# Performance work log

Measured on AMD Instinct MI355X. Metric: run time of the kernel, lower is better.

## Reference

```python
import jax, jax.numpy as jnp
import numpy as np

# Levi-Civita tensor for the 1e x 1e -> 1e CG path (component normalization: eps/sqrt(2))
_e = np.zeros((3, 3, 3), dtype=np.float32)
_e[0, 1, 2] = _e[1, 2, 0] = _e[2, 0, 1] = 1.0
_e[0, 2, 1] = _e[2, 1, 0] = _e[1, 0, 2] = -1.0
EPS = jnp.asarray(_e)

B = 400000
M1S, M1V = 16, 8    # site irreps: 16x0e + 8x1e
MES, MEV = 4, 4     # edge irreps: 4x0e + 4x1e


def _split(x, mul_s, mul_v):
    # flat e3nn layout: scalars first, then vectors (xyz blocks)
    return x[:, :mul_s], x[:, mul_s:].reshape(x.shape[0], mul_v, 3)


def _fctp(x0, x1, y0, y1, W00, W11_0, W01, W10, W11_1):
    """FullyConnectedTensorProduct over irreps {0e,1e} x {0e,1e} -> {0e,1e}.
    x0:[B,u], x1:[B,u,3], y0:[B,v], y1:[B,v,3]."""
    fan0 = W00.shape[0] * W00.shape[1] + W11_0.shape[0] * W11_0.shape[1]
    out0 = (jnp.einsum('bu,bv,uvw->bw', x0, y0, W00)
            + jnp.einsum('bui,bvi,uvw->bw', x1, y1, W11_0) / np.sqrt(3.0)) / np.sqrt(fan0)
    fan1 = (W01.shape[0] * W01.shape[1] + W10.shape[0] * W10.shape[1]
            + W11_1.shape[0] * W11_1.shape[1])
    cross = jnp.einsum('bui,bvj,ijk->buvk', x1, y1, EPS)  # [B,u,v,3]
    out1 = (jnp.einsum('bu,bvi,uvw->bwi', x0, y1, W01)
            + jnp.einsum('bui,bv,uvw->bwi', x1, y0, W10)
            + jnp.einsum('buvk,uvw->bwk', cross, W11_1) / np.sqrt(2.0)) / np.sqrt(fan1)
    return out0, out1


def _forward(site1, site2, edge,
             W1_00, W1_11_0, W1_01, W1_10, W1_11_1,
             W2_00, W2_11_0, W2_01, W2_10, W2_11_1,
             W3_00, W3_11):
    x0, x1 = _split(site1, M1S, M1V)
    y0, y1 = _split(site2, M1S, M1V)
    # node-node tensor product -> 32x0e + 16x1e
    t0, t1 = _fctp(x0, x1, y0, y1, W1_00, W1_11_0, W1_01, W1_10, W1_11_1)
    e0, e1 = _split(edge, MES, MEV)
    # node-node-edge tensor product -> 64x0e + 32x1e
    u0, u1 = _fctp(t0, t1, e0, e1, W2_00, W2_11_0, W2_01, W2_10, W2_11_1)
    # Gate: 32 scalars (silu) | 32 gates (sigmoid) gating 32x1e
    s = jax.nn.silu(u0[:, :32])
    g = jax.nn.sigmoid(u0[:, 32:])
    v = u1 * g[:, :, None]
    # TensorSquare -> 1x0e (component normalization)
    fan = W3_00.shape[0] * W3_00.shape[1] + W3_11.shape[0] * W3_11.shape[1]
    out = (jnp.einsum('bu,bv,uvw->bw', s, s, W3_00)
           + jnp.einsum('bui,bvi,uvw->bw', v, v, W3_11) / np.sqrt(3.0)) / np.sqrt(fan)
    return out


def setup_inputs() -> dict:
    key = jax.random.key(0)
    ks = jax.random.split(key, 16)
    f32 = jnp.float32
    return {
        'site1': jax.random.normal(ks[0], (B, M1S + 3 * M1V), f32),
        'site2': jax.random.normal(ks[1], (B, M1S + 3 * M1V), f32),
        'edge': jax.random.normal(ks[2], (B, MES + 3 * MEV), f32),
        'W1_00': jax.random.normal(ks[3], (16, 16, 32), f32),
        'W1_11_0': jax.random.normal(ks[4], (8, 8, 32), f32),
        'W1_01': jax.random.normal(ks[5], (16, 8, 16), f32),
        'W1_10': jax.random.normal(ks[6], (8, 16, 16), f32),
        'W1_11_1': jax.random.normal(ks[7], (8, 8, 16), f32),
        'W2_00': jax.random.normal(ks[8], (32, 4, 64), f32),
        'W2_11_0': jax.random.normal(ks[9], (16, 4, 64), f32),
        'W2_01': jax.random.normal(ks[10], (32, 4, 32), f32),
        'W2_10': jax.random.normal(ks[11], (16, 4, 32), f32),
        'W2_11_1': jax.random.normal(ks[12], (16, 4, 32), f32),
        'W3_00': jax.random.normal(ks[13], (32, 32, 1), f32),
        'W3_11': jax.random.normal(ks[14], (32, 32, 1), f32),
    }


def reference(site1, site2, edge,
              W1_00, W1_11_0, W1_01, W1_10, W1_11_1,
              W2_00, W2_11_0, W2_01, W2_10, W2_11_1,
              W3_00, W3_11):
    return _forward(site1, site2, edge,
                    W1_00, W1_11_0, W1_01, W1_10, W1_11_1,
                    W2_00, W2_11_0, W2_01, W2_10, W2_11_1,
                    W3_00, W3_11)
```

## Files before the change

### kernel.cpp

```cpp
#include <hip/hip_runtime.h>


#define TPB 128

__device__ __forceinline__ float sigf(float x) {
    return 1.0f / (1.0f + __expf(-x));
}

__global__ __launch_bounds__(TPB, 2)
void intersite_fused(const float* __restrict__ site1,
                     const float* __restrict__ site2,
                     const float* __restrict__ edge,
                     const float* __restrict__ W1_00,
                     const float* __restrict__ W1_11_0,
                     const float* __restrict__ W1_01,
                     const float* __restrict__ W1_10,
                     const float* __restrict__ W1_11_1,
                     const float* __restrict__ W2_00,
                     const float* __restrict__ W2_11_0,
                     const float* __restrict__ W2_01,
                     const float* __restrict__ W2_10,
                     const float* __restrict__ W2_11_1,
                     const float* __restrict__ W3_00,
                     const float* __restrict__ W3_11,
                     float* __restrict__ out, int B)
{
    __shared__ float lds[80 * TPB];
    const int t = threadIdx.x;
    const int b = blockIdx.x * TPB + t;
    if (b >= B) return;

#define LDSF(f) lds[(f) * TPB + t]

    const float inv_s3   = 0.57735026918962576f;
    const float inv_s2   = 0.70710678118654752f;
    const float inv_s320 = 0.05590169943749474f;
    const float inv_s192 = 0.07216878364870323f;
    const float inv_s256 = 0.0625f;
    const float inv_s2048= 0.02209708691207961f;

    {
        const float4* p1 = (const float4*)(site1 + (size_t)b * 40);
        #pragma unroll
        for (int q = 0; q < 10; ++q) {
            float4 r = p1[q];
            LDSF(q*4+0) = r.x; LDSF(q*4+1) = r.y;
            LDSF(q*4+2) = r.z; LDSF(q*4+3) = r.w;
        }
        const float4* p2 = (const float4*)(site2 + (size_t)b * 40);
        #pragma unroll
        for (int q = 0; q < 10; ++q) {
            float4 r = p2[q];
            LDSF(40+q*4+0) = r.x; LDSF(40+q*4+1) = r.y;
            LDSF(40+q*4+2) = r.z; LDSF(40+q*4+3) = r.w;
        }
    }
    float e0[4], e1[12];
    {
        const float4* pe = (const float4*)(edge + (size_t)b * 16);
        float4 r0 = pe[0], r1 = pe[1], r2 = pe[2], r3 = pe[3];
        e0[0]=r0.x; e0[1]=r0.y; e0[2]=r0.z; e0[3]=r0.w;
        e1[0]=r1.x; e1[1]=r1.y; e1[2]=r1.z; e1[3]=r1.w;
        e1[4]=r2.x; e1[5]=r2.y; e1[6]=r2.z; e1[7]=r2.w;
        e1[8]=r3.x; e1[9]=r3.y; e1[10]=r3.z; e1[11]=r3.w;
    }

    float t0[32];
    #pragma unroll
    for (int k = 0; k < 32; ++k) t0[k] = 0.0f;

    #pragma unroll 1
    for (int uv = 0; uv < 256; ++uv) {
        float f = LDSF(uv >> 4) * LDSF(40 + (uv & 15));
        const float* w = W1_00 + uv * 32;
        #pragma unroll
        for (int k = 0; k < 32; ++k) t0[k] = fmaf(f, w[k], t0[k]);
    }
    #pragma unroll 1
    for (int uv = 0; uv < 64; ++uv) {
        int u = uv >> 3, v = uv & 7;
        float d =          LDSF(16+u*3)   * LDSF(56+v*3);
        d = fmaf(LDSF(17+u*3), LDSF(57+v*3), d);
        d = fmaf(LDSF(18+u*3), LDSF(58+v*3), d);
        d *= inv_s3;
        const float* w = W1_11_0 + uv * 32;
        #pragma unroll
        for (int k = 0; k < 32; ++k) t0[k] = fmaf(d, w[k], t0[k]);
    }
    #pragma unroll
    for (int k = 0; k < 32; ++k) t0[k] *= inv_s320;

    float t1[48];
    #pragma unroll
    for (int j = 0; j < 48; ++j) t1[j] = 0.0f;

    {
        float yr[24];
        #pragma unroll
        for (int v = 0; v < 8; ++v)
            #pragma unroll
            for (int i = 0; i < 3; ++i) yr[v*3+i] = LDSF(56 + v*3 + i);
        #pragma unroll
        for (int wc = 0; wc < 2; ++wc) {
            float A[64];
            #pragma unroll
            for (int j = 0; j < 64; ++j) A[j] = 0.0f;
            #pragma unroll 1
            for (int u = 0; u < 16; ++u) {
                float xu = LDSF(u);
                const float* w = W1_01 + u*128 + wc*8;
                #pragma unroll
                for (int v = 0; v < 8; ++v)
                    #pragma unroll
                    for (int k = 0; k < 8; ++k)
                        A[v*8+k] = fmaf(xu, w[v*16+k], A[v*8+k]);
            }
            #pragma unroll
            for (int v = 0; v < 8; ++v)
                #pragma unroll
                for (int k = 0; k < 8; ++k)
                    #pragma unroll
                    for (int i = 0; i < 3; ++i)
                        t1[(wc*8+k)*3+i] = fmaf(A[v*8+k], yr[v*3+i], t1[(wc*8+k)*3+i]);
        }
    }
    {
        float xr[24];
        #pragma unroll
        for (int u = 0; u < 8; ++u)
            #pragma unroll
            for (int i = 0; i < 3; ++i) xr[u*3+i] = LDSF(16 + u*3 + i);
        #pragma unroll
        for (int wc = 0; wc < 2; ++wc) {
            float Bm[64];
            #pragma unroll
            for (int j = 0; j < 64; ++j) Bm[j] = 0.0f;
            #pragma unroll 1
            for (int v = 0; v < 16; ++v) {
                float yv = LDSF(40 + v);
                const float* w = W1_10 + v*16 + wc*8;
                #pragma unroll
                for (int u = 0; u < 8; ++u)
                    #pragma unroll
                    for (int k = 0; k < 8; ++k)
                        Bm[u*8+k] = fmaf(yv, w[u*256+k], Bm[u*8+k]);
            }
            #pragma unroll
            for (int u = 0; u < 8; ++u)
                #pragma unroll
                for (int k = 0; k < 8; ++k)
                    #pragma unroll
                    for (int i = 0; i < 3; ++i)
                        t1[(wc*8+k)*3+i] = fmaf(Bm[u*8+k], xr[u*3+i], t1[(wc*8+k)*3+i]);
        }
    }
    #pragma unroll 1
    for (int uv = 0; uv < 64; ++uv) {
        int u = uv >> 3, v = uv & 7;
        float ax = LDSF(16+u*3), ay = LDSF(17+u*3), az = LDSF(18+u*3);
        float bx = LDSF(56+v*3), by = LDSF(57+v*3), bz = LDSF(58+v*3);
        float cx = (ay*bz - az*by) * inv_s2;
        float cy = (az*bx - ax*bz) * inv_s2;
        float cz = (ax*by - ay*bx) * inv_s2;
        const float* w = W1_11_1 + uv * 16;
        #pragma unroll
        for (int k = 0; k < 16; ++k) {
            t1[k*3+0] = fmaf(cx, w[k], t1[k*3+0]);
            t1[k*3+1] = fmaf(cy, w[k], t1[k*3+1]);
            t1[k*3+2] = fmaf(cz, w[k], t1[k*3+2]);
        }
    }
    #pragma unroll
    for (int j = 0; j < 48; ++j) t1[j] *= inv_s320;

    #pragma unroll
    for (int k = 0; k < 32; ++k) LDSF(k) = t0[k];
    #pragma unroll
    for (int j = 0; j < 48; ++j) LDSF(32 + j) = t1[j];

    float u1[96];
    #pragma unroll
    for (int j = 0; j < 96; ++j) u1[j] = 0.0f;

    #pragma unroll
    for (int wc = 0; wc < 2; ++wc) {
        float A2[64];
        #pragma unroll
        for (int j = 0; j < 64; ++j) A2[j] = 0.0f;
        #pragma unroll 1
        for (int u = 0; u < 32; ++u) {
            float tu = LDSF(u);
            const float* w = W2_01 + u*128 + wc*16;
            #pragma unroll
            for (int v = 0; v < 4; ++v)
                #pragma unroll
                for (int k = 0; k < 16; ++k)
                    A2[v*16+k] = fmaf(tu, w[v*32+k], A2[v*16+k]);
        }
        #pragma unroll
        for (int v = 0; v < 4; ++v)
            #pragma unroll
            for (int k = 0; k < 16; ++k)
                #pragma unroll
                for (int i = 0; i < 3; ++i)
                    u1[(wc*16+k)*3+i] = fmaf(A2[v*16+k], e1[v*3+i], u1[(wc*16+k)*3+i]);
    }
    #pragma unroll 1
    for (int u = 0; u < 16; ++u) {
        float a0 = LDSF(32+u*3), a1 = LDSF(33+u*3), a2 = LDSF(34+u*3);
        #pragma unroll
        for (int v = 0; v < 4; ++v) {
            const float* w = W2_10 + u*128 + v*32;
            float f0 = a0*e0[v], f1 = a1*e0[v], f2 = a2*e0[v];
            #pragma unroll
            for (int k = 0; k < 32; ++k) {
                u1[k*3+0] = fmaf(f0, w[k], u1[k*3+0]);
                u1[k*3+1] = fmaf(f1, w[k], u1[k*3+1]);
                u1[k*3+2] = fmaf(f2, w[k], u1[k*3+2]);
            }
        }
    }
    #pragma unroll 1
    for (int u = 0; u < 16; ++u) {
        float ax = LDSF(32+u*3), ay = LDSF(33+u*3), az = LDSF(34+u*3);
        #pragma unroll
        for (int v = 0; v < 4; ++v) {
            float bx = e1[v*3], by = e1[v*3+1], bz = e1[v*3+2];
            float cx = (ay*bz - az*by) * inv_s2;
            float cy = (az*bx - ax*bz) * inv_s2;
            float cz = (ax*by - ay*bx) * inv_s2;
            const float* w = W2_11_1 + u*128 + v*32;
            #pragma unroll
            for (int k = 0; k < 32; ++k) {
                u1[k*3+0] = fmaf(cx, w[k], u1[k*3+0]);
                u1[k*3+1] = fmaf(cy, w[k], u1[k*3+1]);
                u1[k*3+2] = fmaf(cz, w[k], u1[k*3+2]);
            }
        }
    }
    float u0[64];
    #pragma unroll
    for (int k = 0; k < 64; ++k) u0[k] = 0.0f;
    #pragma unroll 1
    for (int u = 0; u < 32; ++u) {
        float tu = LDSF(u);
        #pragma unroll
        for (int v = 0; v < 4; ++v) {
            float f = tu * e0[v];
            const float* w = W2_00 + u*256 + v*64;
            #pragma unroll
            for (int k = 0; k < 64; ++k) u0[k] = fmaf(f, w[k], u0[k]);
        }
    }
    #pragma unroll 1
    for (int u = 0; u < 16; ++u) {
        float a0 = LDSF(32+u*3), a1 = LDSF(33+u*3), a2 = LDSF(34+u*3);
        #pragma unroll
        for (int v = 0; v < 4; ++v) {
            float d = (a0*e1[v*3] + a1*e1[v*3+1] + a2*e1[v*3+2]) * inv_s3;
            const float* w = W2_11_0 + u*256 + v*64;
            #pragma unroll
            for (int k = 0; k < 64; ++k) u0[k] = fmaf(d, w[k], u0[k]);
        }
    }
    #pragma unroll
    for (int k = 0; k < 64; ++k) u0[k] *= inv_s192;
    #pragma unroll
    for (int j = 0; j < 96; ++j) u1[j] *= inv_s256;

    #pragma unroll
    for (int k = 0; k < 32; ++k) {
        float x = u0[k];
        LDSF(k) = x * sigf(x);
    }
    #pragma unroll
    for (int wv = 0; wv < 32; ++wv) {
        float gw = sigf(u0[32 + wv]);
        u1[wv*3+0] *= gw;  u1[wv*3+1] *= gw;  u1[wv*3+2] *= gw;
    }

    float acc0 = 0.0f, acc1 = 0.0f;
    {
        float zs[32];
        #pragma unroll
        for (int k = 0; k < 32; ++k) zs[k] = 0.0f;
        #pragma unroll 1
        for (int u = 0; u < 32; ++u) {
            float su = LDSF(u);
            const float* wa = W3_00 + u*32;
            #pragma unroll
            for (int k = 0; k < 32; ++k) zs[k] = fmaf(su, wa[k], zs[k]);
        }
        #pragma unroll
        for (int k = 0; k < 32; ++k) acc0 = fmaf(zs[k], LDSF(k), acc0);
    }
    #pragma unroll
    for (int i = 0; i < 3; ++i) {
        #pragma unroll
        for (int wv = 0; wv < 32; ++wv) LDSF(32 + wv) = u1[wv*3 + i];
        float zv[32];
        #pragma unroll
        for (int k = 0; k < 32; ++k) zv[k] = 0.0f;
        #pragma unroll 1
        for (int u = 0; u < 32; ++u) {
            float vu = LDSF(32 + u);
            const float* wb = W3_11 + u*32;
            #pragma unroll
            for (int k = 0; k < 32; ++k) zv[k] = fmaf(vu, wb[k], zv[k]);
        }
        #pragma unroll
        for (int k = 0; k < 32; ++k) acc1 = fmaf(zv[k], LDSF(32 + k), acc1);
    }

    out[b] = (acc0 + acc1 * inv_s3) * inv_s2048;
#undef LDSF
}

extern "C" void kernel_launch(void* const* d_in, const int* in_sizes, int n_in,
                              void* d_out, int out_size, void* d_ws, size_t ws_size,
                              hipStream_t stream)
{
    const float* site1   = (const float*)d_in[0];
    const float* site2   = (const float*)d_in[1];
    const float* edge    = (const float*)d_in[2];
    const float* W1_00   = (const float*)d_in[3];
    const float* W1_11_0 = (const float*)d_in[4];
    const float* W1_01   = (const float*)d_in[5];
    const float* W1_10   = (const float*)d_in[6];
    const float* W1_11_1 = (const float*)d_in[7];
    const float* W2_00   = (const float*)d_in[8];
    const float* W2_11_0 = (const float*)d_in[9];
    const float* W2_01   = (const float*)d_in[10];
    const float* W2_10   = (const float*)d_in[11];
    const float* W2_11_1 = (const float*)d_in[12];
    const float* W3_00   = (const float*)d_in[13];
    const float* W3_11   = (const float*)d_in[14];
    float* out = (float*)d_out;

    const int B = in_sizes[0] / 40;
    dim3 grid((B + TPB - 1) / TPB), block(TPB);
    hipLaunchKernelGGL(intersite_fused, grid, block, 0, stream,
                       site1, site2, edge,
                       W1_00, W1_11_0, W1_01, W1_10, W1_11_1,
                       W2_00, W2_11_0, W2_01, W2_10, W2_11_1,
                       W3_00, W3_11, out, B);
}
```

Baseline: 1.384 ms.

## Split each sample's output channels across four threads with shared LDS staging

Each sample is now processed by four cooperating threads, each owning a quarter of the output channels in every tensor-product stage. Intermediates go through a per-sample LDS row, with barriers between stages, and a shuffle reduction forms the final scalar. Inputs are loaded cooperatively with coalesced float4 reads. This cuts per-thread register arrays (u1 goes from 96 to 24 floats), which should allow higher occupancy (launch bounds raised to 3) and more parallelism. The cost is redundant per-sample scalar work in each thread and extra LDS traffic and synchronisation.

```diff
diff --git a/kernel.cpp b/kernel.cpp
--- a/kernel.cpp
+++ b/kernel.cpp
@@ -2,12 +2,14 @@
 
 
 #define TPB 128
+#define SPB 32
+#define STRIDE 180
 
 __device__ __forceinline__ float sigf(float x) {
     return 1.0f / (1.0f + __expf(-x));
 }
 
-__global__ __launch_bounds__(TPB, 2)
+__global__ __launch_bounds__(TPB, 3)
 void intersite_fused(const float* __restrict__ site1,
                      const float* __restrict__ site2,
                      const float* __restrict__ edge,
@@ -25,12 +27,13 @@
                      const float* __restrict__ W3_11,
                      float* __restrict__ out, int B)
 {
-    __shared__ float lds[80 * TPB];
-    const int t = threadIdx.x;
-    const int b = blockIdx.x * TPB + t;
-    if (b >= B) return;
-
-#define LDSF(f) lds[(f) * TPB + t]
+    __shared__ float lds[SPB * STRIDE];
+    const int t  = threadIdx.x;
+    const int q  = t & 3;
+    const int sL = t >> 2;
+    const int sg = blockIdx.x * SPB + sL;
+
+#define L(f) lds[sL * STRIDE + (f)]
 
     const float inv_s3   = 0.57735026918962576f;
     const float inv_s2   = 0.70710678118654752f;
@@ -40,280 +43,300 @@
     const float inv_s2048= 0.02209708691207961f;
 
     {
-        const float4* p1 = (const float4*)(site1 + (size_t)b * 40);
-        #pragma unroll
-        for (int q = 0; q < 10; ++q) {
-            float4 r = p1[q];
-            LDSF(q*4+0) = r.x; LDSF(q*4+1) = r.y;
-            LDSF(q*4+2) = r.z; LDSF(q*4+3) = r.w;
-        }
-        const float4* p2 = (const float4*)(site2 + (size_t)b * 40);
-        #pragma unroll
-        for (int q = 0; q < 10; ++q) {
-            float4 r = p2[q];
-            LDSF(40+q*4+0) = r.x; LDSF(40+q*4+1) = r.y;
-            LDSF(40+q*4+2) = r.z; LDSF(40+q*4+3) = r.w;
-        }
-    }
-    float e0[4], e1[12];
-    {
-        const float4* pe = (const float4*)(edge + (size_t)b * 16);
-        float4 r0 = pe[0], r1 = pe[1], r2 = pe[2], r3 = pe[3];
-        e0[0]=r0.x; e0[1]=r0.y; e0[2]=r0.z; e0[3]=r0.w;
-        e1[0]=r1.x; e1[1]=r1.y; e1[2]=r1.z; e1[3]=r1.w;
-        e1[4]=r2.x; e1[5]=r2.y; e1[6]=r2.z; e1[7]=r2.w;
-        e1[8]=r3.x; e1[9]=r3.y; e1[10]=r3.z; e1[11]=r3.w;
-    }
-
-    float t0[32];
-    #pragma unroll
-    for (int k = 0; k < 32; ++k) t0[k] = 0.0f;
-
-    #pragma unroll 1
-    for (int uv = 0; uv < 256; ++uv) {
-        float f = LDSF(uv >> 4) * LDSF(40 + (uv & 15));
-        const float* w = W1_00 + uv * 32;
-        #pragma unroll
-        for (int k = 0; k < 32; ++k) t0[k] = fmaf(f, w[k], t0[k]);
-    }
-    #pragma unroll 1
-    for (int uv = 0; uv < 64; ++uv) {
-        int u = uv >> 3, v = uv & 7;
-        float d =          LDSF(16+u*3)   * LDSF(56+v*3);
-        d = fmaf(LDSF(17+u*3), LDSF(57+v*3), d);
-        d = fmaf(LDSF(18+u*3), LDSF(58+v*3), d);
-        d *= inv_s3;
-        const float* w = W1_11_0 + uv * 32;
-        #pragma unroll
-        for (int k = 0; k < 32; ++k) t0[k] = fmaf(d, w[k], t0[k]);
-    }
-    #pragma unroll
-    for (int k = 0; k < 32; ++k) t0[k] *= inv_s320;
-
-    float t1[48];
-    #pragma unroll
-    for (int j = 0; j < 48; ++j) t1[j] = 0.0f;
-
-    {
-        float yr[24];
-        #pragma unroll
-        for (int v = 0; v < 8; ++v)
-            #pragma unroll
-            for (int i = 0; i < 3; ++i) yr[v*3+i] = LDSF(56 + v*3 + i);
-        #pragma unroll
-        for (int wc = 0; wc < 2; ++wc) {
-            float A[64];
-            #pragma unroll
-            for (int j = 0; j < 64; ++j) A[j] = 0.0f;
-            #pragma unroll 1
-            for (int u = 0; u < 16; ++u) {
-                float xu = LDSF(u);
-                const float* w = W1_01 + u*128 + wc*8;
-                #pragma unroll
-                for (int v = 0; v < 8; ++v)
-                    #pragma unroll
-                    for (int k = 0; k < 8; ++k)
-                        A[v*8+k] = fmaf(xu, w[v*16+k], A[v*8+k]);
-            }
-            #pragma unroll
-            for (int v = 0; v < 8; ++v)
-                #pragma unroll
-                for (int k = 0; k < 8; ++k)
-                    #pragma unroll
-                    for (int i = 0; i < 3; ++i)
-                        t1[(wc*8+k)*3+i] = fmaf(A[v*8+k], yr[v*3+i], t1[(wc*8+k)*3+i]);
-        }
-    }
-    {
-        float xr[24];
-        #pragma unroll
-        for (int u = 0; u < 8; ++u)
-            #pragma unroll
-            for (int i = 0; i < 3; ++i) xr[u*3+i] = LDSF(16 + u*3 + i);
-        #pragma unroll
-        for (int wc = 0; wc < 2; ++wc) {
-            float Bm[64];
-            #pragma unroll
-            for (int j = 0; j < 64; ++j) Bm[j] = 0.0f;
-            #pragma unroll 1
-            for (int v = 0; v < 16; ++v) {
-                float yv = LDSF(40 + v);
-                const float* w = W1_10 + v*16 + wc*8;
-                #pragma unroll
-                for (int u = 0; u < 8; ++u)
-                    #pragma unroll
-                    for (int k = 0; k < 8; ++k)
-                        Bm[u*8+k] = fmaf(yv, w[u*256+k], Bm[u*8+k]);
-            }
-            #pragma unroll
-            for (int u = 0; u < 8; ++u)
-                #pragma unroll
-                for (int k = 0; k < 8; ++k)
-                    #pragma unroll
-                    for (int i = 0; i < 3; ++i)
-                        t1[(wc*8+k)*3+i] = fmaf(Bm[u*8+k], xr[u*3+i], t1[(wc*8+k)*3+i]);
-        }
-    }
-    #pragma unroll 1
-    for (int uv = 0; uv < 64; ++uv) {
-        int u = uv >> 3, v = uv & 7;
-        float ax = LDSF(16+u*3), ay = LDSF(17+u*3), az = LDSF(18+u*3);
-        float bx = LDSF(56+v*3), by = LDSF(57+v*3), bz = LDSF(58+v*3);
-        float cx = (ay*bz - az*by) * inv_s2;
-        float cy = (az*bx - ax*bz) * inv_s2;
-        float cz = (ax*by - ay*bx) * inv_s2;
-        const float* w = W1_11_1 + uv * 16;
-        #pragma unroll
-        for (int k = 0; k < 16; ++k) {
-            t1[k*3+0] = fmaf(cx, w[k], t1[k*3+0]);
-            t1[k*3+1] = fmaf(cy, w[k], t1[k*3+1]);
-            t1[k*3+2] = fmaf(cz, w[k], t1[k*3+2]);
-        }
-    }
-    #pragma unroll
-    for (int j = 0; j < 48; ++j) t1[j] *= inv_s320;
-
-    #pragma unroll
-    for (int k = 0; k < 32; ++k) LDSF(k) = t0[k];
-    #pragma unroll
-    for (int j = 0; j < 48; ++j) LDSF(32 + j) = t1[j];
-
-    float u1[96];
-    #pragma unroll
-    for (int j = 0; j < 96; ++j) u1[j] = 0.0f;
-
-    #pragma unroll
-    for (int wc = 0; wc < 2; ++wc) {
-        float A2[64];
-        #pragma unroll
-        for (int j = 0; j < 64; ++j) A2[j] = 0.0f;
-        #pragma unroll 1
-        for (int u = 0; u < 32; ++u) {
-            float tu = LDSF(u);
-            const float* w = W2_01 + u*128 + wc*16;
-            #pragma unroll
-            for (int v = 0; v < 4; ++v)
-                #pragma unroll
-                for (int k = 0; k < 16; ++k)
-                    A2[v*16+k] = fmaf(tu, w[v*32+k], A2[v*16+k]);
-        }
-        #pragma unroll
-        for (int v = 0; v < 4; ++v)
-            #pragma unroll
-            for (int k = 0; k < 16; ++k)
-                #pragma unroll
-                for (int i = 0; i < 3; ++i)
-                    u1[(wc*16+k)*3+i] = fmaf(A2[v*16+k], e1[v*3+i], u1[(wc*16+k)*3+i]);
-    }
+        const float4* g1 = (const float4*)site1;
+        const float4* g2 = (const float4*)site2;
+        const int blk0 = blockIdx.x * SPB * 10;
+        #pragma unroll
+        for (int rr = 0; rr < 3; ++rr) {
+            int r = t + rr * TPB;
+            if (r < SPB * 10) {
+                int G = blk0 + r;
+                if (G * 4 < B * 40) {
+                    int smp = r / 10, f = (r % 10) * 4;
+                    float4 a = g1[G];
+                    float* p = &lds[smp * STRIDE + f];
+                    p[0]=a.x; p[1]=a.y; p[2]=a.z; p[3]=a.w;
+                    float4 c = g2[G];
+                    float* p2 = &lds[smp * STRIDE + 40 + f];
+                    p2[0]=c.x; p2[1]=c.y; p2[2]=c.z; p2[3]=c.w;
+                }
+            }
+        }
+        const float4* ge = (const float4*)edge;
+        int r = t;
+        int G = blockIdx.x * SPB * 4 + r;
+        if (G * 4 < B * 16) {
+            int smp = r / 4, f = 80 + (r % 4) * 4;
+            float4 a = ge[G];
+            float* p = &lds[smp * STRIDE + f];
+            p[0]=a.x; p[1]=a.y; p[2]=a.z; p[3]=a.w;
+        }
+    }
+    __syncthreads();
+
+    float y0r[16];
+    #pragma unroll
+    for (int v = 0; v < 16; ++v) y0r[v] = L(40 + v);
+    float y1r[24];
+    #pragma unroll
+    for (int v = 0; v < 8; ++v)
+        #pragma unroll
+        for (int i = 0; i < 3; ++i) y1r[v*3+i] = L(56 + v*3 + i);
+
+    float t0R[8];
+    #pragma unroll
+    for (int k = 0; k < 8; ++k) t0R[k] = 0.0f;
+
     #pragma unroll 1
     for (int u = 0; u < 16; ++u) {
-        float a0 = LDSF(32+u*3), a1 = LDSF(33+u*3), a2 = LDSF(34+u*3);
-        #pragma unroll
-        for (int v = 0; v < 4; ++v) {
-            const float* w = W2_10 + u*128 + v*32;
-            float f0 = a0*e0[v], f1 = a1*e0[v], f2 = a2*e0[v];
-            #pragma unroll
-            for (int k = 0; k < 32; ++k) {
-                u1[k*3+0] = fmaf(f0, w[k], u1[k*3+0]);
-                u1[k*3+1] = fmaf(f1, w[k], u1[k*3+1]);
-                u1[k*3+2] = fmaf(f2, w[k], u1[k*3+2]);
-            }
-        }
-    }
+        float xu = L(u);
+        const float* w = W1_00 + u*512 + 8*q;
+        #pragma unroll
+        for (int v = 0; v < 16; ++v) {
+            float f = xu * y0r[v];
+            #pragma unroll
+            for (int k = 0; k < 8; ++k) t0R[k] = fmaf(f, w[v*32+k], t0R[k]);
+        }
+    }
+
+    float t1v[12];
+    #pragma unroll
+    for (int j = 0; j < 12; ++j) t1v[j] = 0.0f;
+
     #pragma unroll 1
-    for (int u = 0; u < 16; ++u) {
-        float ax = LDSF(32+u*3), ay = LDSF(33+u*3), az = LDSF(34+u*3);
-        #pragma unroll
-        for (int v = 0; v < 4; ++v) {
-            float bx = e1[v*3], by = e1[v*3+1], bz = e1[v*3+2];
+    for (int u = 0; u < 8; ++u) {
+        float ax = L(16+u*3), ay = L(17+u*3), az = L(18+u*3);
+        const float* w0 = W1_11_0 + u*256 + 8*q;
+        const float* w1 = W1_11_1 + u*128 + 4*q;
+        #pragma unroll
+        for (int v = 0; v < 8; ++v) {
+            float bx = y1r[v*3], by = y1r[v*3+1], bz = y1r[v*3+2];
+            float d = (ax*bx + ay*by + az*bz) * inv_s3;
+            #pragma unroll
+            for (int k = 0; k < 8; ++k) t0R[k] = fmaf(d, w0[v*32+k], t0R[k]);
             float cx = (ay*bz - az*by) * inv_s2;
             float cy = (az*bx - ax*bz) * inv_s2;
             float cz = (ax*by - ay*bx) * inv_s2;
-            const float* w = W2_11_1 + u*128 + v*32;
-            #pragma unroll
-            for (int k = 0; k < 32; ++k) {
-                u1[k*3+0] = fmaf(cx, w[k], u1[k*3+0]);
-                u1[k*3+1] = fmaf(cy, w[k], u1[k*3+1]);
-                u1[k*3+2] = fmaf(cz, w[k], u1[k*3+2]);
-            }
-        }
-    }
-    float u0[64];
-    #pragma unroll
-    for (int k = 0; k < 64; ++k) u0[k] = 0.0f;
+            #pragma unroll
+            for (int k = 0; k < 4; ++k) {
+                float wv = w1[v*16+k];
+                t1v[k*3+0] = fmaf(cx, wv, t1v[k*3+0]);
+                t1v[k*3+1] = fmaf(cy, wv, t1v[k*3+1]);
+                t1v[k*3+2] = fmaf(cz, wv, t1v[k*3+2]);
+            }
+        }
+    }
+    #pragma unroll
+    for (int k = 0; k < 8; ++k) t0R[k] *= inv_s320;
+
+    {
+        float A[32];
+        #pragma unroll
+        for (int j = 0; j < 32; ++j) A[j] = 0.0f;
+        #pragma unroll 1
+        for (int u = 0; u < 16; ++u) {
+            float xu = L(u);
+            const float* w = W1_01 + u*128 + 4*q;
+            #pragma unroll
+            for (int v = 0; v < 8; ++v)
+                #pragma unroll
+                for (int k = 0; k < 4; ++k)
+                    A[v*4+k] = fmaf(xu, w[v*16+k], A[v*4+k]);
+        }
+        #pragma unroll
+        for (int v = 0; v < 8; ++v)
+            #pragma unroll
+            for (int k = 0; k < 4; ++k)
+                #pragma unroll
+                for (int i = 0; i < 3; ++i)
+                    t1v[k*3+i] = fmaf(A[v*4+k], y1r[v*3+i], t1v[k*3+i]);
+    }
+    {
+        float Bm[32];
+        #pragma unroll
+        for (int j = 0; j < 32; ++j) Bm[j] = 0.0f;
+        #pragma unroll 1
+        for (int v = 0; v < 16; ++v) {
+            float yv = y0r[v];
+            const float* w = W1_10 + v*16 + 4*q;
+            #pragma unroll
+            for (int u = 0; u < 8; ++u)
+                #pragma unroll
+                for (int k = 0; k < 4; ++k)
+                    Bm[u*4+k] = fmaf(yv, w[u*256+k], Bm[u*4+k]);
+        }
+        #pragma unroll
+        for (int u = 0; u < 8; ++u) {
+            float ax = L(16+u*3), ay = L(17+u*3), az = L(18+u*3);
+            #pragma unroll
+            for (int k = 0; k < 4; ++k) {
+                float m = Bm[u*4+k];
+                t1v[k*3+0] = fmaf(m, ax, t1v[k*3+0]);
+                t1v[k*3+1] = fmaf(m, ay, t1v[k*3+1]);
+                t1v[k*3+2] = fmaf(m, az, t1v[k*3+2]);
+            }
+        }
+    }
+    #pragma unroll
+    for (int j = 0; j < 12; ++j) t1v[j] *= inv_s320;
+
+    #pragma unroll
+    for (int k = 0; k < 8; ++k) L(96 + 8*q + k) = t0R[k];
+    #pragma unroll
+    for (int k = 0; k < 4; ++k)
+        #pragma unroll
+        for (int i = 0; i < 3; ++i) L(128 + (4*q+k)*3 + i) = t1v[k*3+i];
+    __syncthreads();
+
+    float e0r[4], e1r[12];
+    #pragma unroll
+    for (int v = 0; v < 4; ++v) e0r[v] = L(80 + v);
+    #pragma unroll
+    for (int j = 0; j < 12; ++j) e1r[j] = L(84 + j);
+
+    float u0a[16];
+    #pragma unroll
+    for (int k = 0; k < 16; ++k) u0a[k] = 0.0f;
     #pragma unroll 1
     for (int u = 0; u < 32; ++u) {
-        float tu = LDSF(u);
+        float tu = L(96 + u);
+        const float* wa = W2_00 + u*256 + 16*q;
         #pragma unroll
         for (int v = 0; v < 4; ++v) {
-            float f = tu * e0[v];
-            const float* w = W2_00 + u*256 + v*64;
-            #pragma unroll
-            for (int k = 0; k < 64; ++k) u0[k] = fmaf(f, w[k], u0[k]);
+            float f = tu * e0r[v];
+            #pragma unroll
+            for (int k = 0; k < 16; ++k) u0a[k] = fmaf(f, wa[v*64+k], u0a[k]);
         }
     }
     #pragma unroll 1
     for (int u = 0; u < 16; ++u) {
-        float a0 = LDSF(32+u*3), a1 = LDSF(33+u*3), a2 = LDSF(34+u*3);
+        float ax = L(128+u*3), ay = L(129+u*3), az = L(130+u*3);
+        const float* w0 = W2_11_0 + u*256 + 16*q;
         #pragma unroll
         for (int v = 0; v < 4; ++v) {
-            float d = (a0*e1[v*3] + a1*e1[v*3+1] + a2*e1[v*3+2]) * inv_s3;
-            const float* w = W2_11_0 + u*256 + v*64;
-            #pragma unroll
-            for (int k = 0; k < 64; ++k) u0[k] = fmaf(d, w[k], u0[k]);
-        }
-    }
-    #pragma unroll
-    for (int k = 0; k < 64; ++k) u0[k] *= inv_s192;
-    #pragma unroll
-    for (int j = 0; j < 96; ++j) u1[j] *= inv_s256;
-
-    #pragma unroll
-    for (int k = 0; k < 32; ++k) {
-        float x = u0[k];
-        LDSF(k) = x * sigf(x);
-    }
-    #pragma unroll
-    for (int wv = 0; wv < 32; ++wv) {
-        float gw = sigf(u0[32 + wv]);
-        u1[wv*3+0] *= gw;  u1[wv*3+1] *= gw;  u1[wv*3+2] *= gw;
-    }
-
-    float acc0 = 0.0f, acc1 = 0.0f;
-    {
-        float zs[32];
-        #pragma unroll
-        for (int k = 0; k < 32; ++k) zs[k] = 0.0f;
+            float d = (ax*e1r[v*3] + ay*e1r[v*3+1] + az*e1r[v*3+2]) * inv_s3;
+            #pragma unroll
+            for (int k = 0; k < 16; ++k) u0a[k] = fmaf(d, w0[v*64+k], u0a[k]);
+        }
+    }
+    if (q < 2) {
+        #pragma unroll
+        for (int k = 0; k < 16; ++k) {
+            float x = u0a[k] * inv_s192;
+            L(16*q + k) = x * sigf(x);
+        }
+    } else {
+        #pragma unroll
+        for (int k = 0; k < 16; ++k) {
+            float x = u0a[k] * inv_s192;
+            L(32 + 16*(q-2) + k) = sigf(x);
+        }
+    }
+
+    float u1a[24];
+    #pragma unroll
+    for (int j = 0; j < 24; ++j) u1a[j] = 0.0f;
+    {
+        float A2[32];
+        #pragma unroll
+        for (int j = 0; j < 32; ++j) A2[j] = 0.0f;
         #pragma unroll 1
         for (int u = 0; u < 32; ++u) {
-            float su = LDSF(u);
-            const float* wa = W3_00 + u*32;
-            #pragma unroll
-            for (int k = 0; k < 32; ++k) zs[k] = fmaf(su, wa[k], zs[k]);
-        }
-        #pragma unroll
-        for (int k = 0; k < 32; ++k) acc0 = fmaf(zs[k], LDSF(k), acc0);
-    }
+            float tu = L(96 + u);
+            const float* w = W2_01 + u*128 + 8*q;
+            #pragma unroll
+            for (int v = 0; v < 4; ++v)
+                #pragma unroll
+                for (int k = 0; k < 8; ++k)
+                    A2[v*8+k] = fmaf(tu, w[v*32+k], A2[v*8+k]);
+        }
+        #pragma unroll 1
+        for (int u = 0; u < 16; ++u) {
+            float ax = L(128+u*3), ay = L(129+u*3), az = L(130+u*3);
+            const float* wc = W2_10   + u*128 + 8*q;
+            const float* wx = W2_11_1 + u*128 + 8*q;
+            float C[8];
+            #pragma unroll
+            for (int k = 0; k < 8; ++k) C[k] = 0.0f;
+            #pragma unroll
+            for (int v = 0; v < 4; ++v) {
+                float bx = e1r[v*3], by = e1r[v*3+1], bz = e1r[v*3+2];
+                #pragma unroll
+                for (int k = 0; k < 8; ++k) C[k] = fmaf(e0r[v], wc[v*32+k], C[k]);
+                float cx = (ay*bz - az*by) * inv_s2;
+                float cy = (az*bx - ax*bz) * inv_s2;
+                float cz = (ax*by - ay*bx) * inv_s2;
+                #pragma unroll
+                for (int k = 0; k < 8; ++k) {
+                    float wv = wx[v*32+k];
+                    u1a[k*3+0] = fmaf(cx, wv, u1a[k*3+0]);
+                    u1a[k*3+1] = fmaf(cy, wv, u1a[k*3+1]);
+                    u1a[k*3+2] = fmaf(cz, wv, u1a[k*3+2]);
+                }
+            }
+            #pragma unroll
+            for (int k = 0; k < 8; ++k) {
+                u1a[k*3+0] = fmaf(ax, C[k], u1a[k*3+0]);
+                u1a[k*3+1] = fmaf(ay, C[k], u1a[k*3+1]);
+                u1a[k*3+2] = fmaf(az, C[k], u1a[k*3+2]);
+            }
+        }
+        #pragma unroll
+        for (int v = 0; v < 4; ++v)
+            #pragma unroll
+            for (int k = 0; k < 8; ++k)
+                #pragma unroll
+                for (int i = 0; i < 3; ++i)
+                    u1a[k*3+i] = fmaf(A2[v*8+k], e1r[v*3+i], u1a[k*3+i]);
+    }
+    __syncthreads();
+
+    #pragma unroll
+    for (int k = 0; k < 8; ++k) {
+        float gw = L(32 + 8*q + k) * inv_s256;
+        L(64 + (8*q+k)*3 + 0) = u1a[k*3+0] * gw;
+        L(64 + (8*q+k)*3 + 1) = u1a[k*3+1] * gw;
+        L(64 + (8*q+k)*3 + 2) = u1a[k*3+2] * gw;
+    }
+    __syncthreads();
+
+    float acc0 = 0.0f;
+    {
+        float zs[8];
+        #pragma unroll
+        for (int k = 0; k < 8; ++k) zs[k] = 0.0f;
+        #pragma unroll 1
+        for (int u = 0; u < 32; ++u) {
+            float su = L(u);
+            const float* w = W3_00 + u*32 + 8*q;
+            #pragma unroll
+            for (int k = 0; k < 8; ++k) zs[k] = fmaf(su, w[k], zs[k]);
+        }
+        #pragma unroll
+        for (int k = 0; k < 8; ++k) acc0 = fmaf(zs[k], L(8*q + k), acc0);
+    }
+    float acc1 = 0.0f;
     #pragma unroll
     for (int i = 0; i < 3; ++i) {
-        #pragma unroll
-        for (int wv = 0; wv < 32; ++wv) LDSF(32 + wv) = u1[wv*3 + i];
-        float zv[32];
-        #pragma unroll
-        for (int k = 0; k < 32; ++k) zv[k] = 0.0f;
+        float zv[8];
+        #pragma unroll
+        for (int k = 0; k < 8; ++k) zv[k] = 0.0f;
         #pragma unroll 1
         for (int u = 0; u < 32; ++u) {
-            float vu = LDSF(32 + u);
-            const float* wb = W3_11 + u*32;
-            #pragma unroll
-            for (int k = 0; k < 32; ++k) zv[k] = fmaf(vu, wb[k], zv[k]);
-        }
-        #pragma unroll
-        for (int k = 0; k < 32; ++k) acc1 = fmaf(zv[k], LDSF(32 + k), acc1);
-    }
-
-    out[b] = (acc0 + acc1 * inv_s3) * inv_s2048;
-#undef LDSF
+            float vu = L(64 + u*3 + i);
+            const float* w = W3_11 + u*32 + 8*q;
+            #pragma unroll
+            for (int k = 0; k < 8; ++k) zv[k] = fmaf(vu, w[k], zv[k]);
+        }
+        #pragma unroll
+        for (int k = 0; k < 8; ++k) acc1 = fmaf(zv[k], L(64 + (8*q+k)*3 + i), acc1);
+    }
+
+    float total = (acc0 + acc1 * inv_s3) * inv_s2048;
+    total += __shfl_xor(total, 1);
+    total += __shfl_xor(total, 2);
+    if (q == 0 && sg < B) out[sg] = total;
+#undef L
 }
 
 extern "C" void kernel_launch(void* const* d_in, const int* in_sizes, int n_in,
@@ -338,7 +361,7 @@
     float* out = (float*)d_out;
 
     const int B = in_sizes[0] / 40;
-    dim3 grid((B + TPB - 1) / TPB), block(TPB);
+    dim3 grid((B + SPB - 1) / SPB), block(TPB);
     hipLaunchKernelGGL(intersite_fused, grid, block, 0, stream,
                        site1, site2, edge,
                        W1_00, W1_11_0, W1_01, W1_10, W1_11_1,
```

Result: slower. 2.678 ms (+93.5%).
